# Kernel tuning notes

Measured on AMD Instinct MI355X. Metric: run time of the kernel, lower is better.

## Reference

```python
import jax, jax.numpy as jnp
import numpy as np

B, C, I, E = 2048, 128, 16, 10            # nodes, channels, irreps_in dim (lmax=3 -> 1+3+5+7), elements
M0, K3_0, K2_0, K1_0 = 1, 23, 4, 1        # output 0e: irrep dim, num_paths per correlation order 3/2/1
M1, K3_1, K2_1, K1_1 = 3, 33, 5, 1        # output 1o


def setup_inputs() -> dict:
    key = jax.random.key(0)
    ks = jax.random.split(key, 16)
    g = lambda k, s, sc=1.0: jax.random.normal(k, s, jnp.float32) * sc
    x = g(ks[0], (B, C, I))
    # node_attrs: one-hot chemical element per node
    y = jax.nn.one_hot(jax.random.randint(ks[1], (B,), 0, E), E, dtype=jnp.float32)
    return dict(
        x=x, y=y,
        U3_0=g(ks[2], (M0, I, I, I, K3_0), 0.1), U2_0=g(ks[3], (M0, I, I, K2_0), 0.1),
        U1_0=g(ks[4], (M0, I, K1_0), 0.1),
        W3_0=g(ks[5], (E, K3_0, C), 0.05), W2_0=g(ks[6], (E, K2_0, C), 0.05),
        W1_0=g(ks[7], (E, K1_0, C), 0.05),
        U3_1=g(ks[8], (M1, I, I, I, K3_1), 0.1), U2_1=g(ks[9], (M1, I, I, K2_1), 0.1),
        U1_1=g(ks[10], (M1, I, K1_1), 0.1),
        W3_1=g(ks[11], (E, K3_1, C), 0.05), W2_1=g(ks[12], (E, K2_1, C), 0.05),
        W1_1=g(ks[13], (E, K1_1, C), 0.05),
    )


def _contraction(x, y, U3, U2, U1, W3, W2, W1):
    # MACE Contraction for one output irrep.
    # x: [b,c,i] node features, y: [b,e] one-hot element attrs.
    # main: einsum('...ik,ekc,bci,be->bc...') for correlation order 3
    wy3 = jnp.einsum("ekc,be->bkc", W3, y)                 # per-node selected weights [b,k,c]
    t = jnp.einsum("bkc,bci->bkci", wy3, x)                # [b,k,c,i]
    out = jnp.einsum("mijlk,bkci->bcmjl", U3, t)           # main contraction -> [b,c,m,j,l]
    # order 2: weighting ('...k,ekc,be->bc...') then feature contraction ('bc...i,bci->bc...')
    wy2 = jnp.einsum("ekc,be->bkc", W2, y)
    out = out + jnp.einsum("mjlk,bkc->bcmjl", U2, wy2)
    out = jnp.einsum("bcmji,bci->bcmj", out, x)            # [b,c,m,j]
    # order 1
    wy1 = jnp.einsum("ekc,be->bkc", W1, y)
    out = out + jnp.einsum("mjk,bkc->bcmj", U1, wy1)
    out = jnp.einsum("bcmi,bci->bcm", out, x)              # [b,c,m]
    return out.reshape(out.shape[0], -1)                    # [b, c*m]


def reference(x, y, U3_0, U2_0, U1_0, W3_0, W2_0, W1_0,
              U3_1, U2_1, U1_1, W3_1, W2_1, W1_1):
    out0 = _contraction(x, y, U3_0, U2_0, U1_0, W3_0, W2_0, W1_0)   # 0e -> [b, c]
    out1 = _contraction(x, y, U3_1, U2_1, U1_1, W3_1, W2_1, W1_1)   # 1o -> [b, 3c]
    return jnp.concatenate([out0, out1], axis=-1)                    # [b, 4c]
```

## Files before the change

kernel.cpp:

```cpp
#include <hip/hip_runtime.h>
#include <stdint.h>


#define BN 2048
#define CN 128
#define EN 10

#define NT3 816
#define NT2 136
#define NTT (NT3 + NT2 + 16)
#define K3_0 23
#define K3_1 33
#define K2_0 4
#define K2_1 5

#define U3S0_OFF 0
#define U3S1_OFF (K3_0*NT3)
#define U2S0_OFF (U3S1_OFF + 3*K3_1*NT3)
#define U2S1_OFF (U2S0_OFF + K2_0*NT2)
#define LISTS_OFF (U2S1_OFF + 3*K2_1*NT2)
#define CNT_OFF (LISTS_OFF + EN*BN)

#define PREP_TOT (K3_0*NT3 + 3*K3_1*NT3 + K2_0*NT2 + 3*K2_1*NT2)
#define PREP_BLOCKS ((PREP_TOT + 255) / 256)

typedef float v2f __attribute__((ext_vector_type(2)));
#define FMA2(a, b, c) __builtin_elementwise_fma((a), (b), (c))
static __device__ __forceinline__ v2f splat2(float v) { v2f r; r.x = v; r.y = v; return r; }

__global__ __launch_bounds__(256) void prep_sym(
    const float* __restrict__ U3_0, const float* __restrict__ U2_0,
    const float* __restrict__ U3_1, const float* __restrict__ U2_1,
    const float* __restrict__ yg, float* __restrict__ ws)
{
    const int bid = blockIdx.x, tid = threadIdx.x;
    if (bid < PREP_BLOCKS) {
        const int N0 = K3_0*NT3, N1 = 3*K3_1*NT3, P0 = K2_0*NT2;
        const int it = bid*256 + tid;
        if (it >= PREP_TOT) return;
        if (it < N0 + N1) {
            const float* U3; int m, k, K, t, dst;
            if (it < N0) { U3 = U3_0; K = K3_0; m = 0; k = it / NT3; t = it - k*NT3; dst = U3S0_OFF + it; }
            else { int r = it - N0; U3 = U3_1; K = K3_1; int mk = r / NT3; t = r - mk*NT3;
                   m = mk / K3_1; k = mk - m*K3_1; dst = U3S1_OFF + r; }
            int a = 0, rem = t;
            while (rem >= ((16-a)*(17-a))/2) { rem -= ((16-a)*(17-a))/2; ++a; }
            int b = a;
            while (rem >= 16-b) { rem -= 16-b; ++b; }
            const int cc = b + rem;
            #define AT3(i,j,l) U3[(size_t)(((m*16+(i))*16+(j))*16+(l))*K + k]
            float D = AT3(a,b,cc) + AT3(a,cc,b) + AT3(b,a,cc)
                    + AT3(b,cc,a) + AT3(cc,a,b) + AT3(cc,b,a);
            #undef AT3
            const int eq = (a==b) + (b==cc);
            D *= (eq==2) ? (1.f/6.f) : (eq==1) ? 0.5f : 1.f;
            ws[dst] = D;
        } else {
            const int it2 = it - (N0+N1);
            const float* U2; int m, k, K, pr, dst;
            if (it2 < P0) { U2 = U2_0; K = K2_0; m = 0; k = it2 / NT2; pr = it2 - k*NT2; dst = U2S0_OFF + it2; }
            else { int r = it2 - P0; U2 = U2_1; K = K2_1; int mk = r / NT2; pr = r - mk*NT2;
                   m = mk / K2_1; k = mk - m*K2_1; dst = U2S1_OFF + r; }
            int a = 0, rem = pr;
            while (rem >= 16-a) { rem -= 16-a; ++a; }
            const int b = a + rem;
            float D = U2[(size_t)((m*16+a)*16+b)*K + k]
                    + U2[(size_t)((m*16+b)*16+a)*K + k];
            if (a == b) D *= 0.5f;
            ws[dst] = D;
        }
    } else if (bid < PREP_BLOCKS + EN) {
        const int e = bid - PREP_BLOCKS;
        __shared__ int lcnt;
        if (tid == 0) lcnt = 0;
        __syncthreads();
        int* lists = (int*)(ws + LISTS_OFF);
        for (int b = tid; b < BN; b += 256) {
            if (yg[b*EN + e] > 0.5f) {
                int p = atomicAdd(&lcnt, 1);
                lists[e*BN + p] = b;
            }
        }
        __syncthreads();
        if (tid == 0) ((int*)(ws + CNT_OFF))[e] = lcnt;
    }
}

__global__ __launch_bounds__(128) void sc_fused(
    const float* __restrict__ xg, const float* __restrict__ ws,
    const float* __restrict__ U1_0, const float* __restrict__ U1_1,
    const float* __restrict__ W3_0, const float* __restrict__ W2_0, const float* __restrict__ W1_0,
    const float* __restrict__ W3_1, const float* __restrict__ W2_1, const float* __restrict__ W1_1,
    float* __restrict__ outg)
{
    const int c = blockIdx.x, e = blockIdx.y, tid = threadIdx.x;
    __shared__ float4 Ts[NTT];
    __shared__ v2f xs[16 * 128];

    {
        float w30[K3_0], w31[K3_1];
#pragma unroll
        for (int k = 0; k < K3_0; ++k) w30[k] = W3_0[(e*K3_0 + k)*CN + c];
#pragma unroll
        for (int k = 0; k < K3_1; ++k) w31[k] = W3_1[(e*K3_1 + k)*CN + c];
        const float* u0 = ws + U3S0_OFF;
        const float* u1 = ws + U3S1_OFF;
#pragma unroll 1
        for (int g = tid; g < NT3; g += 128) {
            float a0 = 0.f, a1 = 0.f, a2 = 0.f, a3 = 0.f;
#pragma unroll
            for (int k = 0; k < K3_0; ++k) a0 = fmaf(u0[k*NT3 + g], w30[k], a0);
#pragma unroll
            for (int k = 0; k < K3_1; ++k) {
                const float wv = w31[k];
                a1 = fmaf(u1[k*NT3 + g], wv, a1);
                a2 = fmaf(u1[(K3_1 + k)*NT3 + g], wv, a2);
                a3 = fmaf(u1[(2*K3_1 + k)*NT3 + g], wv, a3);
            }
            Ts[g] = make_float4(a0, a1, a2, a3);
        }
    }
    {
        float w20[K2_0], w21[K2_1];
#pragma unroll
        for (int k = 0; k < K2_0; ++k) w20[k] = W2_0[(e*K2_0 + k)*CN + c];
#pragma unroll
        for (int k = 0; k < K2_1; ++k) w21[k] = W2_1[(e*K2_1 + k)*CN + c];
        const float* u0 = ws + U2S0_OFF;
        const float* u1 = ws + U2S1_OFF;
#pragma unroll 1
        for (int g = tid; g < NT2; g += 128) {
            float a0 = 0.f, a1 = 0.f, a2 = 0.f, a3 = 0.f;
#pragma unroll
            for (int k = 0; k < K2_0; ++k) a0 = fmaf(u0[k*NT2 + g], w20[k], a0);
#pragma unroll
            for (int k = 0; k < K2_1; ++k) {
                const float wv = w21[k];
                a1 = fmaf(u1[k*NT2 + g], wv, a1);
                a2 = fmaf(u1[(K2_1 + k)*NT2 + g], wv, a2);
                a3 = fmaf(u1[(2*K2_1 + k)*NT2 + g], wv, a3);
            }
            Ts[NT3 + g] = make_float4(a0, a1, a2, a3);
        }
    }
    if (tid < 16) {
        const float w10 = W1_0[e*CN + c];
        const float w11 = W1_1[e*CN + c];
        Ts[NT3 + NT2 + tid] = make_float4(U1_0[tid]*w10, U1_1[tid]*w11,
                                          U1_1[16+tid]*w11, U1_1[32+tid]*w11);
    }

    const int* lists = (const int*)(ws + LISTS_OFF) + e*BN;
    const int cnt = ((const int*)(ws + CNT_OFF))[e];
    __syncthreads();

    for (int base = 0; base < cnt; base += 256) {
        const int s0 = base + tid, s1 = base + tid + 128;
        const bool act0 = s0 < cnt, act1 = s1 < cnt;
        const int n0 = lists[act0 ? s0 : 0];
        const int n1 = lists[act1 ? s1 : 0];
        const float4* p0 = (const float4*)(xg + ((size_t)n0*CN + c)*16);
        const float4* p1 = (const float4*)(xg + ((size_t)n1*CN + c)*16);
#pragma unroll
        for (int d = 0; d < 4; ++d) {
            const float4 v0 = p0[d]; const float4 v1 = p1[d];
            v2f w;
            w.x = v0.x; w.y = v1.x; xs[(4*d+0)*128+tid] = w;
            w.x = v0.y; w.y = v1.y; xs[(4*d+1)*128+tid] = w;
            w.x = v0.z; w.y = v1.z; xs[(4*d+2)*128+tid] = w;
            w.x = v0.w; w.y = v1.w; xs[(4*d+3)*128+tid] = w;
        }

        v2f acc0 = splat2(0.f), acc1 = acc0, acc2 = acc0, acc3 = acc0;
        int t3 = 0, t2 = NT3;
#pragma unroll 1
        for (int a = 0; a < 16; ++a) {
            const v2f xa = xs[a*128+tid];
            const float4 t1v = Ts[NT3 + NT2 + a];
            v2f tP0 = splat2(t1v.x), tP1 = splat2(t1v.y),
                tP2 = splat2(t1v.z), tP3 = splat2(t1v.w);
#pragma unroll 1
            for (int b = a; b < 16; ++b) {
                const v2f xb = xs[b*128+tid];
                const float4 c2v = Ts[t2]; ++t2;
                v2f tB0 = splat2(c2v.x), tB1 = splat2(c2v.y),
                    tB2 = splat2(c2v.z), tB3 = splat2(c2v.w);
#pragma unroll 4
                for (int cc = b; cc < 16; ++cc) {
                    const v2f xc = xs[cc*128+tid];
                    const float4 c3v = Ts[t3]; ++t3;
                    tB0 = FMA2(splat2(c3v.x), xc, tB0);
                    tB1 = FMA2(splat2(c3v.y), xc, tB1);
                    tB2 = FMA2(splat2(c3v.z), xc, tB2);
                    tB3 = FMA2(splat2(c3v.w), xc, tB3);
                }
                tP0 = FMA2(tB0, xb, tP0);
                tP1 = FMA2(tB1, xb, tP1);
                tP2 = FMA2(tB2, xb, tP2);
                tP3 = FMA2(tB3, xb, tP3);
            }
            acc0 = FMA2(tP0, xa, acc0);
            acc1 = FMA2(tP1, xa, acc1);
            acc2 = FMA2(tP2, xa, acc2);
            acc3 = FMA2(tP3, xa, acc3);
        }
        if (act0) {
            float* o = outg + (size_t)n0*512;
            o[c] = acc0.x;
            o[128 + c*3 + 0] = acc1.x; o[128 + c*3 + 1] = acc2.x; o[128 + c*3 + 2] = acc3.x;
        }
        if (act1) {
            float* o = outg + (size_t)n1*512;
            o[c] = acc0.y;
            o[128 + c*3 + 0] = acc1.y; o[128 + c*3 + 1] = acc2.y; o[128 + c*3 + 2] = acc3.y;
        }
    }
}

extern "C" void kernel_launch(void* const* d_in, const int* in_sizes, int n_in,
                              void* d_out, int out_size, void* d_ws, size_t ws_size,
                              hipStream_t stream) {
    const float* x = (const float*)d_in[0];
    const float* y = (const float*)d_in[1];
    const float* U3_0 = (const float*)d_in[2];
    const float* U2_0 = (const float*)d_in[3];
    const float* U1_0 = (const float*)d_in[4];
    const float* W3_0 = (const float*)d_in[5];
    const float* W2_0 = (const float*)d_in[6];
    const float* W1_0 = (const float*)d_in[7];
    const float* U3_1 = (const float*)d_in[8];
    const float* U2_1 = (const float*)d_in[9];
    const float* U1_1 = (const float*)d_in[10];
    const float* W3_1 = (const float*)d_in[11];
    const float* W2_1 = (const float*)d_in[12];
    const float* W1_1 = (const float*)d_in[13];
    float* out = (float*)d_out;
    float* ws = (float*)d_ws;

    prep_sym<<<dim3(PREP_BLOCKS + EN), 256, 0, stream>>>(U3_0, U2_0, U3_1, U2_1, y, ws);
    sc_fused<<<dim3(CN, EN), 128, 0, stream>>>(x, ws, U1_0, U1_1,
                                               W3_0, W2_0, W1_0,
                                               W3_1, W2_1, W1_1, out);
}
```

Before: 192.9 us.

## Fuse prep and main kernels into one cooperative launch with grid sync

Merges the symmetrization/list-building prep kernel and the main contraction kernel into a single cooperative kernel, with the prep work spread across the blocks of the main grid and a grid-wide barrier in between. The aim is to remove the second kernel launch and the idle gap between the dependent kernels. It keeps the two-kernel path as a fallback when occupancy or cooperative launch support is insufficient, and adds the cost of a grid-wide sync plus a host-side occupancy query cached in a static.

```diff
diff --git a/kernel.cpp b/kernel.cpp
--- a/kernel.cpp
+++ b/kernel.cpp
@@ -1,5 +1,8 @@
 #include <hip/hip_runtime.h>
+#include <hip/hip_cooperative_groups.h>
 #include <stdint.h>
+
+namespace cg = cooperative_groups;
 
 
 #define BN 2048
@@ -20,6 +23,7 @@
 #define U2S1_OFF (U2S0_OFF + K2_0*NT2)
 #define LISTS_OFF (U2S1_OFF + 3*K2_1*NT2)
 #define CNT_OFF (LISTS_OFF + EN*BN)
+#define WS_NEED_BYTES ((size_t)(CNT_OFF + EN) * 4)
 
 #define PREP_TOT (K3_0*NT3 + 3*K3_1*NT3 + K2_0*NT2 + 3*K2_1*NT2)
 #define PREP_BLOCKS ((PREP_TOT + 255) / 256)
@@ -28,75 +32,55 @@
 #define FMA2(a, b, c) __builtin_elementwise_fma((a), (b), (c))
 static __device__ __forceinline__ v2f splat2(float v) { v2f r; r.x = v; r.y = v; return r; }
 
-__global__ __launch_bounds__(256) void prep_sym(
+static __device__ __forceinline__ void sym_one(
+    int it,
     const float* __restrict__ U3_0, const float* __restrict__ U2_0,
     const float* __restrict__ U3_1, const float* __restrict__ U2_1,
-    const float* __restrict__ yg, float* __restrict__ ws)
-{
-    const int bid = blockIdx.x, tid = threadIdx.x;
-    if (bid < PREP_BLOCKS) {
-        const int N0 = K3_0*NT3, N1 = 3*K3_1*NT3, P0 = K2_0*NT2;
-        const int it = bid*256 + tid;
-        if (it >= PREP_TOT) return;
-        if (it < N0 + N1) {
-            const float* U3; int m, k, K, t, dst;
-            if (it < N0) { U3 = U3_0; K = K3_0; m = 0; k = it / NT3; t = it - k*NT3; dst = U3S0_OFF + it; }
-            else { int r = it - N0; U3 = U3_1; K = K3_1; int mk = r / NT3; t = r - mk*NT3;
-                   m = mk / K3_1; k = mk - m*K3_1; dst = U3S1_OFF + r; }
-            int a = 0, rem = t;
-            while (rem >= ((16-a)*(17-a))/2) { rem -= ((16-a)*(17-a))/2; ++a; }
-            int b = a;
-            while (rem >= 16-b) { rem -= 16-b; ++b; }
-            const int cc = b + rem;
-            #define AT3(i,j,l) U3[(size_t)(((m*16+(i))*16+(j))*16+(l))*K + k]
-            float D = AT3(a,b,cc) + AT3(a,cc,b) + AT3(b,a,cc)
-                    + AT3(b,cc,a) + AT3(cc,a,b) + AT3(cc,b,a);
-            #undef AT3
-            const int eq = (a==b) + (b==cc);
-            D *= (eq==2) ? (1.f/6.f) : (eq==1) ? 0.5f : 1.f;
-            ws[dst] = D;
-        } else {
-            const int it2 = it - (N0+N1);
-            const float* U2; int m, k, K, pr, dst;
-            if (it2 < P0) { U2 = U2_0; K = K2_0; m = 0; k = it2 / NT2; pr = it2 - k*NT2; dst = U2S0_OFF + it2; }
-            else { int r = it2 - P0; U2 = U2_1; K = K2_1; int mk = r / NT2; pr = r - mk*NT2;
-                   m = mk / K2_1; k = mk - m*K2_1; dst = U2S1_OFF + r; }
-            int a = 0, rem = pr;
-            while (rem >= 16-a) { rem -= 16-a; ++a; }
-            const int b = a + rem;
-            float D = U2[(size_t)((m*16+a)*16+b)*K + k]
-                    + U2[(size_t)((m*16+b)*16+a)*K + k];
-            if (a == b) D *= 0.5f;
-            ws[dst] = D;
-        }
-    } else if (bid < PREP_BLOCKS + EN) {
-        const int e = bid - PREP_BLOCKS;
-        __shared__ int lcnt;
-        if (tid == 0) lcnt = 0;
-        __syncthreads();
-        int* lists = (int*)(ws + LISTS_OFF);
-        for (int b = tid; b < BN; b += 256) {
-            if (yg[b*EN + e] > 0.5f) {
-                int p = atomicAdd(&lcnt, 1);
-                lists[e*BN + p] = b;
-            }
-        }
-        __syncthreads();
-        if (tid == 0) ((int*)(ws + CNT_OFF))[e] = lcnt;
-    }
-}
-
-__global__ __launch_bounds__(128) void sc_fused(
+    float* __restrict__ ws)
+{
+    const int N0 = K3_0*NT3, N1 = 3*K3_1*NT3, P0 = K2_0*NT2;
+    if (it < N0 + N1) {
+        const float* U3; int m, k, K, t, dst;
+        if (it < N0) { U3 = U3_0; K = K3_0; m = 0; k = it / NT3; t = it - k*NT3; dst = U3S0_OFF + it; }
+        else { int r = it - N0; U3 = U3_1; K = K3_1; int mk = r / NT3; t = r - mk*NT3;
+               m = mk / K3_1; k = mk - m*K3_1; dst = U3S1_OFF + r; }
+        int a = 0, rem = t;
+        while (rem >= ((16-a)*(17-a))/2) { rem -= ((16-a)*(17-a))/2; ++a; }
+        int b = a;
+        while (rem >= 16-b) { rem -= 16-b; ++b; }
+        const int cc = b + rem;
+        #define AT3(i,j,l) U3[(size_t)(((m*16+(i))*16+(j))*16+(l))*K + k]
+        float D = AT3(a,b,cc) + AT3(a,cc,b) + AT3(b,a,cc)
+                + AT3(b,cc,a) + AT3(cc,a,b) + AT3(cc,b,a);
+        #undef AT3
+        const int eq = (a==b) + (b==cc);
+        D *= (eq==2) ? (1.f/6.f) : (eq==1) ? 0.5f : 1.f;
+        ws[dst] = D;
+    } else {
+        const int it2 = it - (N0+N1);
+        const float* U2; int m, k, K, pr, dst;
+        if (it2 < P0) { U2 = U2_0; K = K2_0; m = 0; k = it2 / NT2; pr = it2 - k*NT2; dst = U2S0_OFF + it2; }
+        else { int r = it2 - P0; U2 = U2_1; K = K2_1; int mk = r / NT2; pr = r - mk*NT2;
+               m = mk / K2_1; k = mk - m*K2_1; dst = U2S1_OFF + r; }
+        int a = 0, rem = pr;
+        while (rem >= 16-a) { rem -= 16-a; ++a; }
+        const int b = a + rem;
+        float D = U2[(size_t)((m*16+a)*16+b)*K + k]
+                + U2[(size_t)((m*16+b)*16+a)*K + k];
+        if (a == b) D *= 0.5f;
+        ws[dst] = D;
+    }
+}
+
+static __device__ __forceinline__ void build_and_apply(
     const float* __restrict__ xg, const float* __restrict__ ws,
     const float* __restrict__ U1_0, const float* __restrict__ U1_1,
     const float* __restrict__ W3_0, const float* __restrict__ W2_0, const float* __restrict__ W1_0,
     const float* __restrict__ W3_1, const float* __restrict__ W2_1, const float* __restrict__ W1_1,
-    float* __restrict__ outg)
-{
-    const int c = blockIdx.x, e = blockIdx.y, tid = threadIdx.x;
-    __shared__ float4 Ts[NTT];
-    __shared__ v2f xs[16 * 128];
-
+    float* __restrict__ outg,
+    float4* __restrict__ Ts, v2f* __restrict__ xs,
+    int c, int e, int tid)
+{
     {
         float w30[K3_0], w31[K3_1];
 #pragma unroll
@@ -217,6 +201,85 @@
     }
 }
 
+__global__ __launch_bounds__(128) void sc_all(
+    const float* __restrict__ xg, float* __restrict__ ws,
+    const float* __restrict__ U3_0, const float* __restrict__ U2_0, const float* __restrict__ U1_0,
+    const float* __restrict__ U3_1, const float* __restrict__ U2_1, const float* __restrict__ U1_1,
+    const float* __restrict__ W3_0, const float* __restrict__ W2_0, const float* __restrict__ W1_0,
+    const float* __restrict__ W3_1, const float* __restrict__ W2_1, const float* __restrict__ W1_1,
+    const float* __restrict__ yg, float* __restrict__ outg)
+{
+    const int c = blockIdx.x, e = blockIdx.y, tid = threadIdx.x;
+    __shared__ float4 Ts[NTT];
+    __shared__ v2f xs[16 * 128];
+    __shared__ int lcnt;
+
+    const int gbid = e * CN + c;
+    const int git = gbid * 128 + tid;
+    if (git < PREP_TOT)
+        sym_one(git, U3_0, U2_0, U3_1, U2_1, ws);
+    if (gbid >= 1024 && gbid < 1024 + EN) {
+        const int e0 = gbid - 1024;
+        if (tid == 0) lcnt = 0;
+        __syncthreads();
+        int* lists = (int*)(ws + LISTS_OFF);
+        for (int b = tid; b < BN; b += 128) {
+            if (yg[b*EN + e0] > 0.5f) {
+                int p = atomicAdd(&lcnt, 1);
+                lists[e0*BN + p] = b;
+            }
+        }
+        __syncthreads();
+        if (tid == 0) ((int*)(ws + CNT_OFF))[e0] = lcnt;
+    }
+    __threadfence();
+    cg::this_grid().sync();
+
+    build_and_apply(xg, ws, U1_0, U1_1, W3_0, W2_0, W1_0,
+                    W3_1, W2_1, W1_1, outg, Ts, xs, c, e, tid);
+}
+
+__global__ __launch_bounds__(256) void prep_sym(
+    const float* __restrict__ U3_0, const float* __restrict__ U2_0,
+    const float* __restrict__ U3_1, const float* __restrict__ U2_1,
+    const float* __restrict__ yg, float* __restrict__ ws)
+{
+    const int bid = blockIdx.x, tid = threadIdx.x;
+    if (bid < PREP_BLOCKS) {
+        const int it = bid*256 + tid;
+        if (it >= PREP_TOT) return;
+        sym_one(it, U3_0, U2_0, U3_1, U2_1, ws);
+    } else if (bid < PREP_BLOCKS + EN) {
+        const int e = bid - PREP_BLOCKS;
+        __shared__ int lc;
+        if (tid == 0) lc = 0;
+        __syncthreads();
+        int* lists = (int*)(ws + LISTS_OFF);
+        for (int b = tid; b < BN; b += 256) {
+            if (yg[b*EN + e] > 0.5f) {
+                int p = atomicAdd(&lc, 1);
+                lists[e*BN + p] = b;
+            }
+        }
+        __syncthreads();
+        if (tid == 0) ((int*)(ws + CNT_OFF))[e] = lc;
+    }
+}
+
+__global__ __launch_bounds__(128) void sc_fused(
+    const float* __restrict__ xg, const float* __restrict__ ws,
+    const float* __restrict__ U1_0, const float* __restrict__ U1_1,
+    const float* __restrict__ W3_0, const float* __restrict__ W2_0, const float* __restrict__ W1_0,
+    const float* __restrict__ W3_1, const float* __restrict__ W2_1, const float* __restrict__ W1_1,
+    float* __restrict__ outg)
+{
+    const int c = blockIdx.x, e = blockIdx.y, tid = threadIdx.x;
+    __shared__ float4 Ts[NTT];
+    __shared__ v2f xs[16 * 128];
+    build_and_apply(xg, ws, U1_0, U1_1, W3_0, W2_0, W1_0,
+                    W3_1, W2_1, W1_1, outg, Ts, xs, c, e, tid);
+}
+
 extern "C" void kernel_launch(void* const* d_in, const int* in_sizes, int n_in,
                               void* d_out, int out_size, void* d_ws, size_t ws_size,
                               hipStream_t stream) {
@@ -237,8 +300,35 @@
     float* out = (float*)d_out;
     float* ws = (float*)d_ws;
 
-    prep_sym<<<dim3(PREP_BLOCKS + EN), 256, 0, stream>>>(U3_0, U2_0, U3_1, U2_1, y, ws);
-    sc_fused<<<dim3(CN, EN), 128, 0, stream>>>(x, ws, U1_0, U1_1,
-                                               W3_0, W2_0, W1_0,
-                                               W3_1, W2_1, W1_1, out);
-}
+    static int coop_ok = -1;
+    if (coop_ok < 0) {
+        int dev = 0;
+        hipGetDevice(&dev);
+        hipDeviceProp_t prop{};
+        hipGetDeviceProperties(&prop, dev);
+        int maxb = 0;
+        hipError_t qe = hipOccupancyMaxActiveBlocksPerMultiprocessor(
+            &maxb, (const void*)sc_all, 128, 0);
+        const int need = (CN * EN + prop.multiProcessorCount - 1) /
+                         (prop.multiProcessorCount > 0 ? prop.multiProcessorCount : 1);
+        coop_ok = (qe == hipSuccess && prop.cooperativeLaunch && maxb >= need) ? 1 : 0;
+    }
+
+    if (ws_size >= WS_NEED_BYTES && coop_ok == 1) {
+        void* args[] = {
+            (void*)&x, (void*)&ws,
+            (void*)&U3_0, (void*)&U2_0, (void*)&U1_0,
+            (void*)&U3_1, (void*)&U2_1, (void*)&U1_1,
+            (void*)&W3_0, (void*)&W2_0, (void*)&W1_0,
+            (void*)&W3_1, (void*)&W2_1, (void*)&W1_1,
+            (void*)&y, (void*)&out
+        };
+        hipLaunchCooperativeKernel((void*)sc_all, dim3(CN, EN), dim3(128),
+                                   args, 0, stream);
+    } else {
+        prep_sym<<<dim3(PREP_BLOCKS + EN), 256, 0, stream>>>(U3_0, U2_0, U3_1, U2_1, y, ws);
+        sc_fused<<<dim3(CN, EN), 128, 0, stream>>>(x, ws, U1_0, U1_1,
+                                                   W3_0, W2_0, W1_0,
+                                                   W3_1, W2_1, W1_1, out);
+    }
+}
```

New measurement: 192.5 us. No clear change (-0.2%).
